# Kernel tuning notes

Hardware: AMD Instinct MI355X
Metric: run time of the kernel (lower is better)

The kernel has to match this reference:

```python
import jax, jax.numpy as jnp
import numpy as np

N_NODES = 10000
N_EDGES = 160000
BATCH = 16
F_IN = 32          # NODE_EMBED_SIZE
HEADS = 4
HDIM = 4
HC = HEADS * HDIM  # 16
N_LAYERS = 4
OBS_DIM = 100
NUM_OUT = 30
HID = 128
POOL_OUT = 15


def setup_inputs() -> dict:
    key = jax.random.key(0)
    ks = jax.random.split(key, 26)
    s = 0.1
    d = {}
    d["x"] = jax.random.normal(ks[0], (BATCH, N_NODES, F_IN), jnp.float32)
    d["obs"] = jax.random.normal(ks[1], (BATCH, OBS_DIM), jnp.float32)
    d["src"] = jax.random.randint(ks[2], (N_EDGES,), 0, N_NODES)
    d["dst"] = jax.random.randint(ks[3], (N_EDGES,), 0, N_NODES)
    # layer 0 (in=F_IN), layers 1..3 (in=HC) GATv2 params
    d["W0l"] = jax.random.normal(ks[4], (F_IN, HC)) * s
    d["W0r"] = jax.random.normal(ks[5], (F_IN, HC)) * s
    d["b0l"] = jnp.zeros((HC,), jnp.float32)
    d["b0r"] = jnp.zeros((HC,), jnp.float32)
    d["Wl"] = jax.random.normal(ks[6], (N_LAYERS - 1, HC, HC)) * s
    d["Wr"] = jax.random.normal(ks[7], (N_LAYERS - 1, HC, HC)) * s
    d["bl"] = jnp.zeros((N_LAYERS - 1, HC), jnp.float32)
    d["br"] = jnp.zeros((N_LAYERS - 1, HC), jnp.float32)
    d["att"] = jax.random.normal(ks[8], (N_LAYERS, HEADS, HDIM)) * s
    d["bias"] = jnp.zeros((N_LAYERS, HC), jnp.float32)
    # mean-pool aggregator projection to 15
    d["Wp"] = jax.random.normal(ks[9], (HC, POOL_OUT)) * s
    d["bp"] = jnp.zeros((POOL_OUT,), jnp.float32)
    # hybrid policy head: cat([feat15, obs100]) -> 128 -> 128 -> num_outputs
    d["W1"] = jax.random.normal(ks[10], (POOL_OUT + OBS_DIM, HID)) * s
    d["b1"] = jnp.zeros((HID,), jnp.float32)
    d["W2"] = jax.random.normal(ks[11], (HID, HID)) * s
    d["b2"] = jnp.zeros((HID,), jnp.float32)
    d["W3"] = jax.random.normal(ks[12], (HID, NUM_OUT)) * s
    d["b3"] = jnp.zeros((NUM_OUT,), jnp.float32)
    return d


def _gatv2_layer(x, src, dst, Wl, Wr, bl, br, att, bias):
    # x: [B,N,F]; src/dst: [E'] (self loops included); att: [H,C]
    B, N, _ = x.shape
    H, C = att.shape
    xl = (x @ Wl + bl).reshape(B, N, H, C)  # source transform
    xr = (x @ Wr + br).reshape(B, N, H, C)  # target transform
    z = jax.nn.leaky_relu(xl[:, src] + xr[:, dst], negative_slope=0.2)  # [B,E,H,C]
    e = jnp.einsum('behc,hc->ebh', z, att)  # [E,B,H] edge-major for segment ops
    m = jax.lax.stop_gradient(jax.ops.segment_max(e, dst, num_segments=N))
    m = jnp.where(jnp.isfinite(m), m, 0.0)
    ex = jnp.exp(e - m[dst])
    ssum = jax.ops.segment_sum(ex, dst, num_segments=N)
    alpha = ex / (ssum[dst] + 1e-16)  # softmax over incoming edges of dst
    msg = xl[:, src] * jnp.transpose(alpha, (1, 0, 2))[..., None]  # [B,E,H,C]
    out = jax.ops.segment_sum(jnp.transpose(msg, (1, 0, 2, 3)), dst, num_segments=N)
    return jnp.transpose(out, (1, 0, 2, 3)).reshape(B, N, H * C) + bias


def reference(x, obs, src, dst, W0l, W0r, b0l, b0r, Wl, Wr, bl, br, att, bias,
              Wp, bp, W1, b1, W2, b2, W3, b3):
    N = x.shape[1]
    loop = jnp.arange(N, dtype=src.dtype)  # PyG add_self_loops=True
    src_f = jnp.concatenate([src, loop])
    dst_f = jnp.concatenate([dst, loop])
    h = _gatv2_layer(x, src_f, dst_f, W0l, W0r, b0l, b0r, att[0], bias[0])
    for l in range(N_LAYERS - 1):
        h = _gatv2_layer(h, src_f, dst_f, Wl[l], Wr[l], bl[l], br[l], att[l + 1], bias[l + 1])
    feat = h.mean(axis=1) @ Wp + bp  # mean-pool aggregator -> [B,15]
    z1 = jnp.tanh(jnp.concatenate([feat, obs], axis=1) @ W1 + b1)
    z2 = jnp.tanh(z1 @ W2 + b2)
    return z2 @ W3 + b3  # logits [B, NUM_OUT]
```

## Files before the change

### kernel.cpp

```cpp
#include <hip/hip_runtime.h>
#include <hip/hip_fp16.h>
#include <cstdint>
#include <cstddef>

#define NN   10000
#define NE   160000
#define NB   16
#define FIN  32
#define HC   16
#define NH   4
#define HD   4
#define OBSD 100
#define NOUT 30
#define HIDD 128
#define PO   15
#define BCAP 64
#define NBUCKET 64
#define EG   2500

typedef float floatx2 __attribute__((ext_vector_type(2)));

__device__ inline uint32_t pack_fp8x4(float a, float b, float c, float d) {
    int p = __builtin_amdgcn_cvt_pk_fp8_f32(a, b, 0, false);
    p = __builtin_amdgcn_cvt_pk_fp8_f32(c, d, p, true);
    return (uint32_t)p;
}

__device__ inline float4 shfl_xor4(float4 v, int m) {
    float4 r;
    r.x = __shfl_xor(v.x, m, 64);
    r.y = __shfl_xor(v.y, m, 64);
    r.z = __shfl_xor(v.z, m, 64);
    r.w = __shfl_xor(v.w, m, 64);
    return r;
}

__global__ void k_build_xform0(const int* __restrict__ src, const int* __restrict__ dst,
                               int* __restrict__ cnt, int* __restrict__ bucket,
                               const float* __restrict__ x,
                               const float* __restrict__ Wlg, const float* __restrict__ Wrg,
                               const float* __restrict__ blg, const float* __restrict__ brg,
                               uint32_t* __restrict__ xl, __half* __restrict__ xr) {
    int bid = blockIdx.x;
    if (bid < 625) {
        int e = bid * 256 + threadIdx.x;
        if (e < NE) {
            int d = dst[e];
            int p = atomicAdd(&cnt[d], 1);
            if (p < BCAP) bucket[(size_t)d * BCAP + p] = src[e];
        }
        return;
    }
    __shared__ float sWl[FIN * HC], sWr[FIN * HC], sbl[HC], sbr[HC];
    for (int i = threadIdx.x; i < FIN * HC; i += 256) { sWl[i] = Wlg[i]; sWr[i] = Wrg[i]; }
    if (threadIdx.x < HC) { sbl[threadIdx.x] = blg[threadIdx.x]; sbr[threadIdx.x] = brg[threadIdx.x]; }
    __syncthreads();
    int local = bid - 625;
    int b = local / 40;
    int n = (local % 40) * 256 + threadIdx.x;
    if (n >= NN) return;
    const float* xp = x + ((size_t)b * NN + n) * FIN;
    float row[FIN];
#pragma unroll
    for (int f = 0; f < FIN; f++) row[f] = xp[f];
    float al[HC], ar[HC];
#pragma unroll
    for (int c = 0; c < HC; c++) { al[c] = sbl[c]; ar[c] = sbr[c]; }
#pragma unroll
    for (int f = 0; f < FIN; f++) {
        float v = row[f];
#pragma unroll
        for (int c = 0; c < HC; c++) {
            al[c] = fmaf(v, sWl[f * HC + c], al[c]);
            ar[c] = fmaf(v, sWr[f * HC + c], ar[c]);
        }
    }
    uint32_t* xlo = xl + ((size_t)n * NB + b) * 4;
    __half2*  xro = (__half2*)(xr + ((size_t)n * NB + b) * HC);
#pragma unroll
    for (int hh = 0; hh < 4; hh++)
        xlo[hh] = pack_fp8x4(al[hh * 4 + 0], al[hh * 4 + 1], al[hh * 4 + 2], al[hh * 4 + 3]);
#pragma unroll
    for (int c = 0; c < HC; c += 2) xro[c >> 1] = __floats2half2_rn(ar[c], ar[c + 1]);
}

template <int MODE>
__global__ __launch_bounds__(256, 4)
void k_edge_f(const uint32_t* __restrict__ xl, const __half* __restrict__ xr,
              const int* __restrict__ cntg, const int* __restrict__ bucket,
              const float* __restrict__ attg, const float* __restrict__ biasg,
              const float* __restrict__ Wln, const float* __restrict__ Wrn,
              const float* __restrict__ bln, const float* __restrict__ brn,
              uint32_t* __restrict__ xl_o, __half* __restrict__ xr_o,
              float* __restrict__ pool_part) {
    __shared__ float smem[MODE == 2 ? 1024 : 544];
    if (MODE == 1) {
        int t = threadIdx.x;
        smem[t] = Wln[t];
        smem[256 + t] = Wrn[t];
        if (t < HC) { smem[512 + t] = bln[t]; smem[528 + t] = brn[t]; }
        __syncthreads();
    }
    const int tid  = threadIdx.x;
    const int wave = (blockIdx.x * 256 + tid) >> 6;
    const int lane = tid & 63;
    const int n = wave;
    const int h = lane & 3;
    const float4 a4 = *(const float4*)(attg + h * HD);
    const float4 bias4 = *(const float4*)(biasg + h * HD);
    float4 xr4;
    {
        const uint2 xrr = *(const uint2*)(xr + (size_t)n * (NB * HC) + lane * 4);
        float2 p0 = __half22float2(*(const __half2*)&xrr.x);
        float2 p1 = __half22float2(*(const __half2*)&xrr.y);
        xr4 = make_float4(p0.x, p0.y, p1.x, p1.y);
    }
    int cnt = __builtin_amdgcn_readfirstlane(cntg[n]);
    cnt = cnt < BCAP ? cnt : BCAP;
    float4 acc = make_float4(0.f, 0.f, 0.f, 0.f);
    float ssum = 0.f;

#define EDGE_BODY(RAW, M)                                                     \
    {                                                                         \
        floatx2 f0 = __builtin_amdgcn_cvt_pk_f32_fp8((int)(RAW), false);      \
        floatx2 f1 = __builtin_amdgcn_cvt_pk_f32_fp8((int)(RAW), true);       \
        float z0 = f0.x + xr4.x; z0 = fmaxf(z0, 0.2f * z0);                   \
        float z1 = f0.y + xr4.y; z1 = fmaxf(z1, 0.2f * z1);                   \
        float z2 = f1.x + xr4.z; z2 = fmaxf(z2, 0.2f * z2);                   \
        float z3 = f1.y + xr4.w; z3 = fmaxf(z3, 0.2f * z3);                   \
        float e = fmaf(z3, a4.w, fmaf(z2, a4.z, fmaf(z1, a4.y, z0 * a4.x)));  \
        float ex = (M) * __expf(e);                                           \
        ssum += ex;                                                           \
        acc.x = fmaf(ex, f0.x, acc.x);                                        \
        acc.y = fmaf(ex, f0.y, acc.y);                                        \
        acc.z = fmaf(ex, f1.x, acc.z);                                        \
        acc.w = fmaf(ex, f1.y, acc.w);                                        \
    }
#define GATHER(S) xl[(size_t)(S) * 64 + lane]

    { const uint32_t r = GATHER(n); EDGE_BODY(r, 1.0f); }
    if (cnt > 0) {
        const int* brow = bucket + (size_t)n * BCAP;
        int li = lane < cnt ? lane : cnt - 1;
        int vidx = brow[li];
        for (int i = 0; i < cnt; i += 16) {
            uint32_t r[16];
#pragma unroll
            for (int u = 0; u < 16; u++) {
                int e = i + u;
                int ec = e < cnt ? e : cnt - 1;
                int s = __builtin_amdgcn_readlane(vidx, ec);
                r[u] = GATHER(s);
            }
#pragma unroll
            for (int u = 0; u < 16; u++) {
                float m = (i + u < cnt) ? 1.0f : 0.0f;
                EDGE_BODY(r[u], m);
            }
        }
    }
#undef GATHER
#undef EDGE_BODY

    float inv = 1.0f / (ssum + 1e-16f);
    float4 o;
    o.x = fmaf(acc.x, inv, bias4.x);
    o.y = fmaf(acc.y, inv, bias4.y);
    o.z = fmaf(acc.z, inv, bias4.z);
    o.w = fmaf(acc.w, inv, bias4.w);

    if (MODE == 1) {
        float accl[4], accr[4];
#pragma unroll
        for (int cj = 0; cj < 4; cj++) {
            accl[cj] = smem[512 + h * 4 + cj];
            accr[cj] = smem[528 + h * 4 + cj];
        }
#pragma unroll
        for (int m = 0; m < 4; m++) {
            float4 vals = (m == 0) ? o : shfl_xor4(o, m);
            int fbase = ((h ^ m) << 2);
            float vv[4] = {vals.x, vals.y, vals.z, vals.w};
#pragma unroll
            for (int j = 0; j < 4; j++) {
                const float4 wl = *(const float4*)&smem[(fbase + j) * HC + (h << 2)];
                const float4 wr = *(const float4*)&smem[256 + (fbase + j) * HC + (h << 2)];
                float v = vv[j];
                accl[0] = fmaf(v, wl.x, accl[0]);
                accl[1] = fmaf(v, wl.y, accl[1]);
                accl[2] = fmaf(v, wl.z, accl[2]);
                accl[3] = fmaf(v, wl.w, accl[3]);
                accr[0] = fmaf(v, wr.x, accr[0]);
                accr[1] = fmaf(v, wr.y, accr[1]);
                accr[2] = fmaf(v, wr.z, accr[2]);
                accr[3] = fmaf(v, wr.w, accr[3]);
            }
        }
        xl_o[(size_t)n * 64 + lane] = pack_fp8x4(accl[0], accl[1], accl[2], accl[3]);
        __half2* xro = (__half2*)(xr_o + (size_t)n * (NB * HC) + lane * 4);
        xro[0] = __floats2half2_rn(accr[0], accr[1]);
        xro[1] = __floats2half2_rn(accr[2], accr[3]);
    } else {
        *(float4*)&smem[tid * 4] = o;
        __syncthreads();
        if (tid < 64) {
            float4 s0 = *(const float4*)&smem[tid * 4];
            float4 s1v = *(const float4*)&smem[(64 + tid) * 4];
            float4 s2v = *(const float4*)&smem[(128 + tid) * 4];
            float4 s3v = *(const float4*)&smem[(192 + tid) * 4];
            float* dp = pool_part + (blockIdx.x & (NBUCKET - 1)) * 256 + tid * 4;
            atomicAdd(dp + 0, s0.x + s1v.x + s2v.x + s3v.x);
            atomicAdd(dp + 1, s0.y + s1v.y + s2v.y + s3v.y);
            atomicAdd(dp + 2, s0.z + s1v.z + s2v.z + s3v.z);
            atomicAdd(dp + 3, s0.w + s1v.w + s2v.w + s3v.w);
        }
    }
}

__global__ void k_head(const float* __restrict__ pool_part, const float* __restrict__ obs,
                       const float* __restrict__ Wp, const float* __restrict__ bp,
                       const float* __restrict__ W1, const float* __restrict__ b1,
                       const float* __restrict__ W2, const float* __restrict__ b2,
                       const float* __restrict__ W3, const float* __restrict__ b3,
                       float* __restrict__ out) {
    const int b = blockIdx.x;
    const int t = threadIdx.x;
    __shared__ float sPart[64];
    __shared__ float sPool[HC];
    __shared__ float sIn[PO + OBSD];
    __shared__ float s1[HIDD], s2[HIDD];
    if (t < 64) {
        int c = t & 15, q4 = t >> 4;
        float ps = 0.f;
#pragma unroll
        for (int q = q4; q < NBUCKET; q += 4)
            ps += pool_part[q * 256 + b * HC + c];
        sPart[t] = ps;
    }
    __syncthreads();
    if (t < HC) {
        sPool[t] = (sPart[t] + sPart[16 + t] + sPart[32 + t] + sPart[48 + t]) * (1.0f / NN);
    }
    for (int k = t; k < OBSD; k += 256) sIn[PO + k] = obs[b * OBSD + k];
    __syncthreads();
    if (t < PO) {
        float acc = bp[t];
#pragma unroll
        for (int c = 0; c < HC; c++) acc = fmaf(sPool[c], Wp[c * PO + t], acc);
        sIn[t] = acc;
    }
    __syncthreads();
    if (t < HIDD) {
        float acc = b1[t];
        for (int k = 0; k < PO + OBSD; k++) acc = fmaf(sIn[k], W1[k * HIDD + t], acc);
        s1[t] = tanhf(acc);
    }
    __syncthreads();
    if (t < HIDD) {
        float acc = b2[t];
        for (int k = 0; k < HIDD; k++) acc = fmaf(s1[k], W2[k * HIDD + t], acc);
        s2[t] = tanhf(acc);
    }
    __syncthreads();
    if (t < NOUT) {
        float acc = b3[t];
        for (int k = 0; k < HIDD; k++) acc = fmaf(s2[k], W3[k * NOUT + t], acc);
        out[b * NOUT + t] = acc;
    }
}

extern "C" void kernel_launch(void* const* d_in, const int* in_sizes, int n_in,
                              void* d_out, int out_size, void* d_ws, size_t ws_size,
                              hipStream_t stream) {
    const float* x    = (const float*)d_in[0];
    const float* obs  = (const float*)d_in[1];
    const int*   src  = (const int*)d_in[2];
    const int*   dst  = (const int*)d_in[3];
    const float* W0l  = (const float*)d_in[4];
    const float* W0r  = (const float*)d_in[5];
    const float* b0l  = (const float*)d_in[6];
    const float* b0r  = (const float*)d_in[7];
    const float* Wl   = (const float*)d_in[8];
    const float* Wr   = (const float*)d_in[9];
    const float* bl   = (const float*)d_in[10];
    const float* br   = (const float*)d_in[11];
    const float* att  = (const float*)d_in[12];
    const float* bias = (const float*)d_in[13];
    const float* Wp   = (const float*)d_in[14];
    const float* bp   = (const float*)d_in[15];
    const float* W1   = (const float*)d_in[16];
    const float* b1   = (const float*)d_in[17];
    const float* W2   = (const float*)d_in[18];
    const float* b2   = (const float*)d_in[19];
    const float* W3   = (const float*)d_in[20];
    const float* b3   = (const float*)d_in[21];
    float* out = (float*)d_out;

    size_t off = 0;
    auto take = [&](size_t bytes) -> void* {
        void* ptr = (char*)d_ws + off;
        off += (bytes + 255) & ~(size_t)255;
        return ptr;
    };
    int*      cnt       = (int*)take(NN * sizeof(int));
    float*    pool_part = (float*)take(NBUCKET * 256 * sizeof(float));
    int*      bucket    = (int*)take((size_t)NN * BCAP * sizeof(int));
    uint32_t* xlA       = (uint32_t*)take((size_t)NN * 64 * sizeof(uint32_t));
    __half*   xrA       = (__half*)take((size_t)NN * NB * HC * sizeof(__half));
    uint32_t* xlB       = (uint32_t*)take((size_t)NN * 64 * sizeof(uint32_t));
    __half*   xrB       = (__half*)take((size_t)NN * NB * HC * sizeof(__half));

    size_t zspan = (size_t)((char*)(pool_part + NBUCKET * 256) - (char*)cnt);
    hipMemsetAsync(cnt, 0, zspan, stream);

    k_build_xform0<<<625 + 40 * NB, 256, 0, stream>>>(src, dst, cnt, bucket,
                                                      x, W0l, W0r, b0l, b0r, xlA, xrA);

    k_edge_f<1><<<EG, 256, 0, stream>>>(xlA, xrA, cnt, bucket,
                                        att + 0 * 16, bias + 0 * 16,
                                        Wl + 0 * 256, Wr + 0 * 256, bl + 0 * 16, br + 0 * 16,
                                        xlB, xrB, nullptr);
    k_edge_f<1><<<EG, 256, 0, stream>>>(xlB, xrB, cnt, bucket,
                                        att + 1 * 16, bias + 1 * 16,
                                        Wl + 1 * 256, Wr + 1 * 256, bl + 1 * 16, br + 1 * 16,
                                        xlA, xrA, nullptr);
    k_edge_f<1><<<EG, 256, 0, stream>>>(xlA, xrA, cnt, bucket,
                                        att + 2 * 16, bias + 2 * 16,
                                        Wl + 2 * 256, Wr + 2 * 256, bl + 2 * 16, br + 2 * 16,
                                        xlB, xrB, nullptr);
    k_edge_f<2><<<EG, 256, 0, stream>>>(xlB, xrB, cnt, bucket,
                                        att + 3 * 16, bias + 3 * 16,
                                        nullptr, nullptr, nullptr, nullptr,
                                        nullptr, nullptr, pool_part);

    k_head<<<NB, 256, 0, stream>>>(pool_part, obs, Wp, bp, W1, b1, W2, b2, W3, b3, out);
}
```

Baseline: 130.4 us.

## Store xr in fp8, fuse MLP head into last layer, split unmasked edge loop

Three changes. The target transform xr is stored as packed fp8 instead of fp16, halving its bytes. The MLP head is fused into the final edge kernel as extra blocks that spin on a completion counter until all pooling partials are written, which removes one kernel launch. The edge loop is split into full unmasked 16-edge chunks plus a masked 8- or 16-edge tail, cutting wasted gathers and compare work. The risks are lower accuracy from fp8 xr and a deadlock if the head blocks are scheduled before the producer blocks can run.

```diff
diff --git a/kernel.cpp b/kernel.cpp
--- a/kernel.cpp
+++ b/kernel.cpp
@@ -1,5 +1,4 @@
 #include <hip/hip_runtime.h>
-#include <hip/hip_fp16.h>
 #include <cstdint>
 #include <cstddef>
 
@@ -40,7 +39,7 @@
                                const float* __restrict__ x,
                                const float* __restrict__ Wlg, const float* __restrict__ Wrg,
                                const float* __restrict__ blg, const float* __restrict__ brg,
-                               uint32_t* __restrict__ xl, __half* __restrict__ xr) {
+                               uint32_t* __restrict__ xl, uint32_t* __restrict__ xr) {
     int bid = blockIdx.x;
     if (bid < 625) {
         int e = bid * 256 + threadIdx.x;
@@ -76,32 +75,94 @@
         }
     }
     uint32_t* xlo = xl + ((size_t)n * NB + b) * 4;
-    __half2*  xro = (__half2*)(xr + ((size_t)n * NB + b) * HC);
-#pragma unroll
-    for (int hh = 0; hh < 4; hh++)
+    uint32_t* xro = xr + ((size_t)n * NB + b) * 4;
+#pragma unroll
+    for (int hh = 0; hh < 4; hh++) {
         xlo[hh] = pack_fp8x4(al[hh * 4 + 0], al[hh * 4 + 1], al[hh * 4 + 2], al[hh * 4 + 3]);
-#pragma unroll
-    for (int c = 0; c < HC; c += 2) xro[c >> 1] = __floats2half2_rn(ar[c], ar[c + 1]);
+        xro[hh] = pack_fp8x4(ar[hh * 4 + 0], ar[hh * 4 + 1], ar[hh * 4 + 2], ar[hh * 4 + 3]);
+    }
 }
 
 template <int MODE>
 __global__ __launch_bounds__(256, 4)
-void k_edge_f(const uint32_t* __restrict__ xl, const __half* __restrict__ xr,
+void k_edge_f(const uint32_t* __restrict__ xl, const uint32_t* __restrict__ xr,
               const int* __restrict__ cntg, const int* __restrict__ bucket,
               const float* __restrict__ attg, const float* __restrict__ biasg,
               const float* __restrict__ Wln, const float* __restrict__ Wrn,
               const float* __restrict__ bln, const float* __restrict__ brn,
-              uint32_t* __restrict__ xl_o, __half* __restrict__ xr_o,
-              float* __restrict__ pool_part) {
-    __shared__ float smem[MODE == 2 ? 1024 : 544];
+              uint32_t* __restrict__ xl_o, uint32_t* __restrict__ xr_o,
+              float* __restrict__ pool_part, int* __restrict__ done_sub,
+              int* __restrict__ master,
+              const float* __restrict__ obs,
+              const float* __restrict__ Wp, const float* __restrict__ bp,
+              const float* __restrict__ W1, const float* __restrict__ b1,
+              const float* __restrict__ W2, const float* __restrict__ b2,
+              const float* __restrict__ W3, const float* __restrict__ b3,
+              float* __restrict__ out) {
+    __shared__ float smem[1024];
+    const int tid = threadIdx.x;
+
+    if (MODE == 2 && blockIdx.x >= EG) {
+        const int b = blockIdx.x - EG;
+        if (tid == 0) {
+            while (__hip_atomic_load(master, __ATOMIC_RELAXED,
+                                     __HIP_MEMORY_SCOPE_AGENT) < NBUCKET) {
+                __builtin_amdgcn_s_sleep(16);
+            }
+        }
+        __syncthreads();
+        float* sPart = smem;
+        float* sPool = smem + 64;
+        float* sIn   = smem + 80;
+        float* s1a   = smem + 208;
+        float* s2a   = smem + 336;
+        if (tid < 64) {
+            int c = tid & 15, q4 = tid >> 4;
+            float ps = 0.f;
+#pragma unroll
+            for (int q = q4; q < NBUCKET; q += 4)
+                ps += __hip_atomic_load(&pool_part[q * 256 + b * HC + c],
+                                        __ATOMIC_RELAXED, __HIP_MEMORY_SCOPE_AGENT);
+            sPart[tid] = ps;
+        }
+        __syncthreads();
+        if (tid < HC)
+            sPool[tid] = (sPart[tid] + sPart[16 + tid] + sPart[32 + tid] + sPart[48 + tid]) * (1.0f / NN);
+        for (int k = tid; k < OBSD; k += 256) sIn[PO + k] = obs[b * OBSD + k];
+        __syncthreads();
+        if (tid < PO) {
+            float acc = bp[tid];
+#pragma unroll
+            for (int c = 0; c < HC; c++) acc = fmaf(sPool[c], Wp[c * PO + tid], acc);
+            sIn[tid] = acc;
+        }
+        __syncthreads();
+        if (tid < HIDD) {
+            float acc = b1[tid];
+            for (int k = 0; k < PO + OBSD; k++) acc = fmaf(sIn[k], W1[k * HIDD + tid], acc);
+            s1a[tid] = tanhf(acc);
+        }
+        __syncthreads();
+        if (tid < HIDD) {
+            float acc = b2[tid];
+            for (int k = 0; k < HIDD; k++) acc = fmaf(s1a[k], W2[k * HIDD + tid], acc);
+            s2a[tid] = tanhf(acc);
+        }
+        __syncthreads();
+        if (tid < NOUT) {
+            float acc = b3[tid];
+            for (int k = 0; k < HIDD; k++) acc = fmaf(s2a[k], W3[k * NOUT + tid], acc);
+            out[b * NOUT + tid] = acc;
+        }
+        return;
+    }
+
     if (MODE == 1) {
-        int t = threadIdx.x;
-        smem[t] = Wln[t];
-        smem[256 + t] = Wrn[t];
-        if (t < HC) { smem[512 + t] = bln[t]; smem[528 + t] = brn[t]; }
-        __syncthreads();
-    }
-    const int tid  = threadIdx.x;
+        smem[tid] = Wln[tid];
+        smem[256 + tid] = Wrn[tid];
+        if (tid < HC) { smem[512 + tid] = bln[tid]; smem[528 + tid] = brn[tid]; }
+        __syncthreads();
+    }
     const int wave = (blockIdx.x * 256 + tid) >> 6;
     const int lane = tid & 63;
     const int n = wave;
@@ -110,17 +171,17 @@
     const float4 bias4 = *(const float4*)(biasg + h * HD);
     float4 xr4;
     {
-        const uint2 xrr = *(const uint2*)(xr + (size_t)n * (NB * HC) + lane * 4);
-        float2 p0 = __half22float2(*(const __half2*)&xrr.x);
-        float2 p1 = __half22float2(*(const __half2*)&xrr.y);
-        xr4 = make_float4(p0.x, p0.y, p1.x, p1.y);
+        uint32_t xrr = xr[(size_t)n * 64 + lane];
+        floatx2 q0 = __builtin_amdgcn_cvt_pk_f32_fp8((int)xrr, false);
+        floatx2 q1 = __builtin_amdgcn_cvt_pk_f32_fp8((int)xrr, true);
+        xr4 = make_float4(q0.x, q0.y, q1.x, q1.y);
     }
     int cnt = __builtin_amdgcn_readfirstlane(cntg[n]);
     cnt = cnt < BCAP ? cnt : BCAP;
     float4 acc = make_float4(0.f, 0.f, 0.f, 0.f);
     float ssum = 0.f;
 
-#define EDGE_BODY(RAW, M)                                                     \
+#define EDGE_CORE(RAW, EXPR)                                                  \
     {                                                                         \
         floatx2 f0 = __builtin_amdgcn_cvt_pk_f32_fp8((int)(RAW), false);      \
         floatx2 f1 = __builtin_amdgcn_cvt_pk_f32_fp8((int)(RAW), true);       \
@@ -129,38 +190,68 @@
         float z2 = f1.x + xr4.z; z2 = fmaxf(z2, 0.2f * z2);                   \
         float z3 = f1.y + xr4.w; z3 = fmaxf(z3, 0.2f * z3);                   \
         float e = fmaf(z3, a4.w, fmaf(z2, a4.z, fmaf(z1, a4.y, z0 * a4.x)));  \
-        float ex = (M) * __expf(e);                                           \
+        float ex = EXPR;                                                      \
         ssum += ex;                                                           \
         acc.x = fmaf(ex, f0.x, acc.x);                                        \
         acc.y = fmaf(ex, f0.y, acc.y);                                        \
         acc.z = fmaf(ex, f1.x, acc.z);                                        \
         acc.w = fmaf(ex, f1.y, acc.w);                                        \
     }
+#define EDGE_BODY1(RAW)    EDGE_CORE(RAW, __expf(e))
+#define EDGE_BODYM(RAW, M) EDGE_CORE(RAW, (M) * __expf(e))
 #define GATHER(S) xl[(size_t)(S) * 64 + lane]
 
-    { const uint32_t r = GATHER(n); EDGE_BODY(r, 1.0f); }
+    { const uint32_t r = GATHER(n); EDGE_BODY1(r); }
     if (cnt > 0) {
         const int* brow = bucket + (size_t)n * BCAP;
         int li = lane < cnt ? lane : cnt - 1;
         int vidx = brow[li];
-        for (int i = 0; i < cnt; i += 16) {
+        int i = 0;
+        for (; i + 16 <= cnt; i += 16) {
             uint32_t r[16];
 #pragma unroll
             for (int u = 0; u < 16; u++) {
-                int e = i + u;
-                int ec = e < cnt ? e : cnt - 1;
+                int s = __builtin_amdgcn_readlane(vidx, i + u);
+                r[u] = GATHER(s);
+            }
+#pragma unroll
+            for (int u = 0; u < 16; u++) EDGE_BODY1(r[u]);
+        }
+        int rem = cnt - i;
+        if (rem > 8) {
+            uint32_t r[16];
+#pragma unroll
+            for (int u = 0; u < 16; u++) {
+                int e2 = i + u;
+                int ec = e2 < cnt ? e2 : cnt - 1;
                 int s = __builtin_amdgcn_readlane(vidx, ec);
                 r[u] = GATHER(s);
             }
 #pragma unroll
             for (int u = 0; u < 16; u++) {
                 float m = (i + u < cnt) ? 1.0f : 0.0f;
-                EDGE_BODY(r[u], m);
+                EDGE_BODYM(r[u], m);
+            }
+        } else if (rem > 0) {
+            uint32_t r[8];
+#pragma unroll
+            for (int u = 0; u < 8; u++) {
+                int e2 = i + u;
+                int ec = e2 < cnt ? e2 : cnt - 1;
+                int s = __builtin_amdgcn_readlane(vidx, ec);
+                r[u] = GATHER(s);
+            }
+#pragma unroll
+            for (int u = 0; u < 8; u++) {
+                float m = (i + u < cnt) ? 1.0f : 0.0f;
+                EDGE_BODYM(r[u], m);
             }
         }
     }
 #undef GATHER
-#undef EDGE_BODY
+#undef EDGE_BODY1
+#undef EDGE_BODYM
+#undef EDGE_CORE
 
     float inv = 1.0f / (ssum + 1e-16f);
     float4 o;
@@ -197,9 +288,7 @@
             }
         }
         xl_o[(size_t)n * 64 + lane] = pack_fp8x4(accl[0], accl[1], accl[2], accl[3]);
-        __half2* xro = (__half2*)(xr_o + (size_t)n * (NB * HC) + lane * 4);
-        xro[0] = __floats2half2_rn(accr[0], accr[1]);
-        xro[1] = __floats2half2_rn(accr[2], accr[3]);
+        xr_o[(size_t)n * 64 + lane] = pack_fp8x4(accr[0], accr[1], accr[2], accr[3]);
     } else {
         *(float4*)&smem[tid * 4] = o;
         __syncthreads();
@@ -214,58 +303,16 @@
             atomicAdd(dp + 2, s0.z + s1v.z + s2v.z + s3v.z);
             atomicAdd(dp + 3, s0.w + s1v.w + s2v.w + s3v.w);
         }
-    }
-}
-
-__global__ void k_head(const float* __restrict__ pool_part, const float* __restrict__ obs,
-                       const float* __restrict__ Wp, const float* __restrict__ bp,
-                       const float* __restrict__ W1, const float* __restrict__ b1,
-                       const float* __restrict__ W2, const float* __restrict__ b2,
-                       const float* __restrict__ W3, const float* __restrict__ b3,
-                       float* __restrict__ out) {
-    const int b = blockIdx.x;
-    const int t = threadIdx.x;
-    __shared__ float sPart[64];
-    __shared__ float sPool[HC];
-    __shared__ float sIn[PO + OBSD];
-    __shared__ float s1[HIDD], s2[HIDD];
-    if (t < 64) {
-        int c = t & 15, q4 = t >> 4;
-        float ps = 0.f;
-#pragma unroll
-        for (int q = q4; q < NBUCKET; q += 4)
-            ps += pool_part[q * 256 + b * HC + c];
-        sPart[t] = ps;
-    }
-    __syncthreads();
-    if (t < HC) {
-        sPool[t] = (sPart[t] + sPart[16 + t] + sPart[32 + t] + sPart[48 + t]) * (1.0f / NN);
-    }
-    for (int k = t; k < OBSD; k += 256) sIn[PO + k] = obs[b * OBSD + k];
-    __syncthreads();
-    if (t < PO) {
-        float acc = bp[t];
-#pragma unroll
-        for (int c = 0; c < HC; c++) acc = fmaf(sPool[c], Wp[c * PO + t], acc);
-        sIn[t] = acc;
-    }
-    __syncthreads();
-    if (t < HIDD) {
-        float acc = b1[t];
-        for (int k = 0; k < PO + OBSD; k++) acc = fmaf(sIn[k], W1[k * HIDD + t], acc);
-        s1[t] = tanhf(acc);
-    }
-    __syncthreads();
-    if (t < HIDD) {
-        float acc = b2[t];
-        for (int k = 0; k < HIDD; k++) acc = fmaf(s1[k], W2[k * HIDD + t], acc);
-        s2[t] = tanhf(acc);
-    }
-    __syncthreads();
-    if (t < NOUT) {
-        float acc = b3[t];
-        for (int k = 0; k < HIDD; k++) acc = fmaf(s2[k], W3[k * NOUT + t], acc);
-        out[b * NOUT + t] = acc;
+        if (tid == 0) {
+            asm volatile("s_waitcnt vmcnt(0)" ::: "memory");
+            int s = blockIdx.x & 63;
+            int quota = (s < (EG & 63)) ? (EG / 64 + 1) : (EG / 64);
+            int old = __hip_atomic_fetch_add(&done_sub[s], 1, __ATOMIC_RELAXED,
+                                             __HIP_MEMORY_SCOPE_AGENT);
+            if (old == quota - 1)
+                __hip_atomic_fetch_add(master, 1, __ATOMIC_RELAXED,
+                                       __HIP_MEMORY_SCOPE_AGENT);
+        }
     }
 }
 
@@ -304,13 +351,15 @@
     };
     int*      cnt       = (int*)take(NN * sizeof(int));
     float*    pool_part = (float*)take(NBUCKET * 256 * sizeof(float));
+    int*      done_sub  = (int*)take(64 * sizeof(int));
+    int*      master    = (int*)take(64 * sizeof(int));
     int*      bucket    = (int*)take((size_t)NN * BCAP * sizeof(int));
     uint32_t* xlA       = (uint32_t*)take((size_t)NN * 64 * sizeof(uint32_t));
-    __half*   xrA       = (__half*)take((size_t)NN * NB * HC * sizeof(__half));
+    uint32_t* xrA       = (uint32_t*)take((size_t)NN * 64 * sizeof(uint32_t));
     uint32_t* xlB       = (uint32_t*)take((size_t)NN * 64 * sizeof(uint32_t));
-    __half*   xrB       = (__half*)take((size_t)NN * NB * HC * sizeof(__half));
-
-    size_t zspan = (size_t)((char*)(pool_part + NBUCKET * 256) - (char*)cnt);
+    uint32_t* xrB       = (uint32_t*)take((size_t)NN * 64 * sizeof(uint32_t));
+
+    size_t zspan = (size_t)((char*)(master + 64) - (char*)cnt);
     hipMemsetAsync(cnt, 0, zspan, stream);
 
     k_build_xform0<<<625 + 40 * NB, 256, 0, stream>>>(src, dst, cnt, bucket,
@@ -319,19 +368,25 @@
     k_edge_f<1><<<EG, 256, 0, stream>>>(xlA, xrA, cnt, bucket,
                                         att + 0 * 16, bias + 0 * 16,
                                         Wl + 0 * 256, Wr + 0 * 256, bl + 0 * 16, br + 0 * 16,
-                                        xlB, xrB, nullptr);
+                                        xlB, xrB, nullptr, nullptr, nullptr,
+                                        nullptr, nullptr, nullptr, nullptr, nullptr,
+                                        nullptr, nullptr, nullptr, nullptr, nullptr);
     k_edge_f<1><<<EG, 256, 0, stream>>>(xlB, xrB, cnt, bucket,
                                         att + 1 * 16, bias + 1 * 16,
                                         Wl + 1 * 256, Wr + 1 * 256, bl + 1 * 16, br + 1 * 16,
-                                        xlA, xrA, nullptr);
+                                        xlA, xrA, nullptr, nullptr, nullptr,
+                                        nullptr, nullptr, nullptr, nullptr, nullptr,
+                                        nullptr, nullptr, nullptr, nullptr, nullptr);
     k_edge_f<1><<<EG, 256, 0, stream>>>(xlA, xrA, cnt, bucket,
                                         att + 2 * 16, bias + 2 * 16,
                                         Wl + 2 * 256, Wr + 2 * 256, bl + 2 * 16, br + 2 * 16,
-                                        xlB, xrB, nullptr);
-    k_edge_f<2><<<EG, 256, 0, stream>>>(xlB, xrB, cnt, bucket,
-                                        att + 3 * 16, bias + 3 * 16,
-                                        nullptr, nullptr, nullptr, nullptr,
-                                        nullptr, nullptr, pool_part);
-
-    k_head<<<NB, 256, 0, stream>>>(pool_part, obs, Wp, bp, W1, b1, W2, b2, W3, b3, out);
-}
+                                        xlB, xrB, nullptr, nullptr, nullptr,
+                                        nullptr, nullptr, nullptr, nullptr, nullptr,
+                                        nullptr, nullptr, nullptr, nullptr, nullptr);
+    k_edge_f<2><<<EG + NB, 256, 0, stream>>>(xlB, xrB, cnt, bucket,
+                                             att + 3 * 16, bias + 3 * 16,
+                                             nullptr, nullptr, nullptr, nullptr,
+                                             nullptr, nullptr, pool_part, done_sub,
+                                             master, obs, Wp, bp, W1, b1, W2, b2,
+                                             W3, b3, out);
+}
```

Measured after the change: 130.1 us. Within noise of the previous version (-0.2%).
